# Performance work log

Measured on AMD Instinct MI355X. Metric: run time of the kernel, lower is better.

## Reference

```python
import jax, jax.numpy as jnp
import numpy as np

N_IN, N_OUT, K, G = 128, 128, 3, 8
BATCH = 512
GRID_MIN, GRID_MAX = -1.0, 1.0
EDGES = N_IN * N_OUT


def setup_inputs() -> dict:
    key = jax.random.key(0)
    k1, k2 = jax.random.split(key)
    # inputs inside the grid range so splines are active
    x = jax.random.uniform(k1, (BATCH, N_IN), dtype=jnp.float32,
                           minval=GRID_MIN, maxval=GRID_MAX)
    # per-edge extended uniform knot vector: G+2K+1 points (k extra on each side)
    h = (GRID_MAX - GRID_MIN) / G
    knots_1d = jnp.linspace(GRID_MIN - K * h, GRID_MAX + K * h,
                            G + 2 * K + 1, dtype=jnp.float32)
    knots = jnp.broadcast_to(knots_1d, (EDGES, G + 2 * K + 1))
    c_basis = (jax.random.normal(k2, (EDGES, G + K), dtype=jnp.float32) * 0.1)
    c_spl = jnp.ones((N_OUT, N_IN), jnp.float32)
    c_res = jnp.ones((N_OUT, N_IN), jnp.float32)
    bias = jnp.zeros((N_OUT,), jnp.float32)
    return {"x": x, "knots": knots, "c_basis": c_basis,
            "c_spl": c_spl, "c_res": c_res, "bias": bias}


def _extend(x):
    # (batch, n_in) -> (edges, batch) with edge index = o*n_in + i
    batch = x.shape[0]
    return jnp.broadcast_to(x[:, None, :], (batch, N_OUT, N_IN)).reshape(batch, EDGES).T


def _basis(x, knots):
    # Cox-de Boor recursion; returns (edges, G+K, batch)
    x_ext = _extend(x)                   # (edges, batch)
    grid = knots[:, :, None]             # (edges, G+2K+1, 1)
    x_in = x_ext[:, None, :]             # (edges, 1, batch)
    b = ((x_in >= grid[:, :-1]) & (x_in < grid[:, 1:])).astype(jnp.float32)
    for order in range(1, K + 1):
        left = (x_in - grid[:, :-(order + 1)]) / (grid[:, order:-1] - grid[:, :-(order + 1)])
        right = (grid[:, order + 1:] - x_in) / (grid[:, order + 1:] - grid[:, 1:-order])
        b = left * b[:, :-1] + right * b[:, 1:]
    return b


def reference(x, knots, c_basis, c_spl, c_res, bias):
    batch = x.shape[0]
    bi = _basis(x, knots)                           # (edges, G+K, batch)
    spl = jnp.einsum('eg,egb->eb', c_basis, bi).T   # (batch, edges)
    y = c_spl.reshape(1, EDGES) * spl
    x_ext = _extend(x).T                            # (batch, edges)
    y = y + c_res.reshape(1, EDGES) * jax.nn.silu(x_ext)
    y = jnp.sum(y.reshape(batch, N_OUT, N_IN), axis=2) + bias
    return y
```

## Files before the change

kernel.cpp:

```cpp
#include <hip/hip_runtime.h>
#include <math.h>

#define N_IN  128
#define N_OUT 128
#define BATCH 512
#define NK    11
#define TBV   16
#define TOV   16
#define KTOT  1536
#define ASTR  1544

typedef float f32x4  __attribute__((ext_vector_type(4)));
typedef short bf16x8 __attribute__((ext_vector_type(8)));
typedef unsigned long long u64;

__device__ __forceinline__ unsigned short f2bf(float f) {
    unsigned u = __float_as_uint(f);
    u += 0x7FFFu + ((u >> 16) & 1u);
    return (unsigned short)(u >> 16);
}

__global__ __launch_bounds__(128) void w_pack(
    const float* __restrict__ cbasis, const float* __restrict__ cspl,
    const float* __restrict__ cres, unsigned short* __restrict__ w2)
{
    const int e = blockIdx.x * 128 + threadIdx.x;
    const float s = cspl[e];
    const float* src = cbasis + (size_t)e * NK;
    unsigned short h[12];
    #pragma unroll
    for (int g = 0; g < NK; ++g) h[g] = f2bf(s * src[g]);
    h[11] = f2bf(cres[e]);
    unsigned d[6];
    #pragma unroll
    for (int j = 0; j < 6; ++j)
        d[j] = (unsigned)h[2 * j] | ((unsigned)h[2 * j + 1] << 16);
    unsigned short* dst = w2 + (size_t)e * 12;
    *(uint2*)(dst)     = make_uint2(d[0], d[1]);
    *(uint2*)(dst + 4) = make_uint2(d[2], d[3]);
    *(uint2*)(dst + 8) = make_uint2(d[4], d[5]);
}

__global__ __launch_bounds__(512) void kan_kernel(
    const float* __restrict__ x,
    const unsigned short* __restrict__ w2,
    const float* __restrict__ bias,
    float* __restrict__ y)
{
    __shared__ short sA[TBV * ASTR];
    __shared__ float sAcc[8 * 256];

    const int b0 = blockIdx.x * TBV;
    const int o0 = blockIdx.y * TOV;
    const int t  = threadIdx.x;
    const int w  = t >> 6;
    const int l  = t & 63;
    const int mn = l & 15;
    const int kq = (l >> 4) * 8;

    const unsigned short* wb = w2 + (size_t)(o0 + mn) * KTOT + w * 192 + kq;
    bf16x8 wf[6];
    #pragma unroll
    for (int s = 0; s < 6; ++s)
        wf[s] = *(const bf16x8*)(wb + s * 32);

    float xv[4];
    #pragma unroll
    for (int it = 0; it < 4; ++it) {
        const int p = t + it * 512;
        xv[it] = x[(b0 + (p >> 7)) * N_IN + (p & 127)];
    }
    #pragma unroll
    for (int it = 0; it < 4; ++it) {
        const int p = t + it * 512;
        const int b = p >> 7, i = p & 127;
        const float v = xv[it];
        const float u = (v + 1.75f) * 4.0f;
        float jf = floorf(u);
        jf = fminf(fmaxf(jf, 3.0f), 10.0f);
        const float tt = u - jf;
        const float omt = 1.0f - tt;
        const float t2 = tt * tt, t3 = t2 * tt;
        const float B0 = omt * omt * omt * (1.0f / 6.0f);
        const float B1 = (3.0f * t3 - 6.0f * t2 + 4.0f) * (1.0f / 6.0f);
        const float B2 = (-3.0f * t3 + 3.0f * t2 + 3.0f * tt + 1.0f) * (1.0f / 6.0f);
        const float B3 = t3 * (1.0f / 6.0f);
        const int base = (int)jf - 3;
        const float sig = 1.0f / (1.0f + __expf(-v));
        const u64 v4 = (u64)f2bf(B0) | ((u64)f2bf(B1) << 16)
                     | ((u64)f2bf(B2) << 32) | ((u64)f2bf(B3) << 48);
        const int sh = base * 16;
        u64 q0, q1, q2;
        if (sh < 64) {
            q0 = v4 << sh;
            q1 = sh ? (v4 >> (64 - sh)) : 0ull;
            q2 = 0ull;
        } else {
            q0 = 0ull;
            q1 = v4 << (sh - 64);
            q2 = (sh > 64) ? (v4 >> (128 - sh)) : 0ull;
        }
        q2 |= (u64)f2bf(v * sig) << 48;
        u64* dst = (u64*)&sA[b * ASTR + i * 12];
        dst[0] = q0; dst[1] = q1; dst[2] = q2;
    }
    __syncthreads();

    f32x4 acc = {0.f, 0.f, 0.f, 0.f};
    const short* aB = &sA[mn * ASTR + w * 192 + kq];
    #pragma unroll
    for (int s = 0; s < 6; ++s) {
        bf16x8 af = *(const bf16x8*)(aB + s * 32);
        acc = __builtin_amdgcn_mfma_f32_16x16x32_bf16(af, wf[s], acc, 0, 0, 0);
    }

    #pragma unroll
    for (int r = 0; r < 4; ++r)
        sAcc[w * 256 + ((l >> 4) * 4 + r) * 16 + mn] = acc[r];
    __syncthreads();
    if (t < 256) {
        const int m2 = t >> 4, n2 = t & 15;
        float sum = bias[o0 + n2];
        #pragma unroll
        for (int ww = 0; ww < 8; ++ww) sum += sAcc[ww * 256 + t];
        y[(b0 + m2) * N_OUT + (o0 + n2)] = sum;
    }
}

extern "C" void kernel_launch(void* const* d_in, const int* in_sizes, int n_in,
                              void* d_out, int out_size, void* d_ws, size_t ws_size,
                              hipStream_t stream) {
    const float* x      = (const float*)d_in[0];
    const float* cbasis = (const float*)d_in[2];
    const float* cspl   = (const float*)d_in[3];
    const float* cres   = (const float*)d_in[4];
    const float* bias   = (const float*)d_in[5];
    float* y = (float*)d_out;
    unsigned short* w2 = (unsigned short*)d_ws;

    w_pack<<<128, 128, 0, stream>>>(cbasis, cspl, cres, w2);
    dim3 grid(BATCH / TBV, N_OUT / TOV);
    kan_kernel<<<grid, 512, 0, stream>>>(x, w2, bias, y);
}
```

Measured before the change: 67.11 us.

## Precompute spline basis activations once in pack kernel instead of per output tile

Moves the B-spline basis and SiLU evaluation of x out of the GEMM kernel into the packing kernel, which writes a global bf16 activation matrix alongside the packed weights. Previously each of the 8 output-tile columns recomputed the basis for its batch tile in shared memory; now the GEMM kernel loads both operands directly from global into registers with no shared staging or barrier. This removes redundant transcendental work and a sync, at the cost of an extra global write/read of the activation matrix (about 1.5 MB).

```diff
diff --git a/kernel.cpp b/kernel.cpp
--- a/kernel.cpp
+++ b/kernel.cpp
@@ -8,7 +8,6 @@
 #define TBV   16
 #define TOV   16
 #define KTOT  1536
-#define ASTR  1544
 
 typedef float f32x4  __attribute__((ext_vector_type(4)));
 typedef short bf16x8 __attribute__((ext_vector_type(8)));
@@ -20,61 +19,30 @@
     return (unsigned short)(u >> 16);
 }
 
-__global__ __launch_bounds__(128) void w_pack(
-    const float* __restrict__ cbasis, const float* __restrict__ cspl,
-    const float* __restrict__ cres, unsigned short* __restrict__ w2)
+__global__ __launch_bounds__(256) void pack_kernel(
+    const float* __restrict__ x,      const float* __restrict__ cbasis,
+    const float* __restrict__ cspl,   const float* __restrict__ cres,
+    unsigned short* __restrict__ w2,  unsigned short* __restrict__ a2)
 {
-    const int e = blockIdx.x * 128 + threadIdx.x;
-    const float s = cspl[e];
-    const float* src = cbasis + (size_t)e * NK;
-    unsigned short h[12];
-    #pragma unroll
-    for (int g = 0; g < NK; ++g) h[g] = f2bf(s * src[g]);
-    h[11] = f2bf(cres[e]);
-    unsigned d[6];
-    #pragma unroll
-    for (int j = 0; j < 6; ++j)
-        d[j] = (unsigned)h[2 * j] | ((unsigned)h[2 * j + 1] << 16);
-    unsigned short* dst = w2 + (size_t)e * 12;
-    *(uint2*)(dst)     = make_uint2(d[0], d[1]);
-    *(uint2*)(dst + 4) = make_uint2(d[2], d[3]);
-    *(uint2*)(dst + 8) = make_uint2(d[4], d[5]);
-}
-
-__global__ __launch_bounds__(512) void kan_kernel(
-    const float* __restrict__ x,
-    const unsigned short* __restrict__ w2,
-    const float* __restrict__ bias,
-    float* __restrict__ y)
-{
-    __shared__ short sA[TBV * ASTR];
-    __shared__ float sAcc[8 * 256];
-
-    const int b0 = blockIdx.x * TBV;
-    const int o0 = blockIdx.y * TOV;
-    const int t  = threadIdx.x;
-    const int w  = t >> 6;
-    const int l  = t & 63;
-    const int mn = l & 15;
-    const int kq = (l >> 4) * 8;
-
-    const unsigned short* wb = w2 + (size_t)(o0 + mn) * KTOT + w * 192 + kq;
-    bf16x8 wf[6];
-    #pragma unroll
-    for (int s = 0; s < 6; ++s)
-        wf[s] = *(const bf16x8*)(wb + s * 32);
-
-    float xv[4];
-    #pragma unroll
-    for (int it = 0; it < 4; ++it) {
-        const int p = t + it * 512;
-        xv[it] = x[(b0 + (p >> 7)) * N_IN + (p & 127)];
-    }
-    #pragma unroll
-    for (int it = 0; it < 4; ++it) {
-        const int p = t + it * 512;
-        const int b = p >> 7, i = p & 127;
-        const float v = xv[it];
+    if (blockIdx.x < 64) {
+        const int e = blockIdx.x * 256 + threadIdx.x;
+        const float s = cspl[e];
+        const float* src = cbasis + (size_t)e * NK;
+        unsigned short h[12];
+        #pragma unroll
+        for (int g = 0; g < NK; ++g) h[g] = f2bf(s * src[g]);
+        h[11] = f2bf(cres[e]);
+        unsigned d[6];
+        #pragma unroll
+        for (int j = 0; j < 6; ++j)
+            d[j] = (unsigned)h[2 * j] | ((unsigned)h[2 * j + 1] << 16);
+        unsigned short* dst = w2 + (size_t)e * 12;
+        *(uint2*)(dst)     = make_uint2(d[0], d[1]);
+        *(uint2*)(dst + 4) = make_uint2(d[2], d[3]);
+        *(uint2*)(dst + 8) = make_uint2(d[4], d[5]);
+    } else {
+        const int p = (blockIdx.x - 64) * 256 + threadIdx.x;
+        const float v = x[p];
         const float u = (v + 1.75f) * 4.0f;
         float jf = floorf(u);
         jf = fminf(fmaxf(jf, 3.0f), 10.0f);
@@ -101,18 +69,40 @@
             q2 = (sh > 64) ? (v4 >> (128 - sh)) : 0ull;
         }
         q2 |= (u64)f2bf(v * sig) << 48;
-        u64* dst = (u64*)&sA[b * ASTR + i * 12];
+        u64* dst = (u64*)(a2 + (size_t)p * 12);
         dst[0] = q0; dst[1] = q1; dst[2] = q2;
     }
-    __syncthreads();
+}
+
+__global__ __launch_bounds__(512) void kan_kernel(
+    const unsigned short* __restrict__ a2,
+    const unsigned short* __restrict__ w2,
+    const float* __restrict__ bias,
+    float* __restrict__ y)
+{
+    __shared__ float sAcc[8 * 256];
+
+    const int b0 = blockIdx.x * TBV;
+    const int o0 = blockIdx.y * TOV;
+    const int t  = threadIdx.x;
+    const int w  = t >> 6;
+    const int l  = t & 63;
+    const int mn = l & 15;
+    const int kq = (l >> 4) * 8;
+
+    const unsigned short* ab = a2 + (size_t)(b0 + mn) * KTOT + w * 192 + kq;
+    const unsigned short* wb = w2 + (size_t)(o0 + mn) * KTOT + w * 192 + kq;
+    bf16x8 af[6], wf[6];
+    #pragma unroll
+    for (int s = 0; s < 6; ++s) {
+        af[s] = *(const bf16x8*)(ab + s * 32);
+        wf[s] = *(const bf16x8*)(wb + s * 32);
+    }
 
     f32x4 acc = {0.f, 0.f, 0.f, 0.f};
-    const short* aB = &sA[mn * ASTR + w * 192 + kq];
     #pragma unroll
-    for (int s = 0; s < 6; ++s) {
-        bf16x8 af = *(const bf16x8*)(aB + s * 32);
-        acc = __builtin_amdgcn_mfma_f32_16x16x32_bf16(af, wf[s], acc, 0, 0, 0);
-    }
+    for (int s = 0; s < 6; ++s)
+        acc = __builtin_amdgcn_mfma_f32_16x16x32_bf16(af[s], wf[s], acc, 0, 0, 0);
 
     #pragma unroll
     for (int r = 0; r < 4; ++r)
@@ -137,8 +127,9 @@
     const float* bias   = (const float*)d_in[5];
     float* y = (float*)d_out;
     unsigned short* w2 = (unsigned short*)d_ws;
+    unsigned short* a2 = (unsigned short*)((char*)d_ws + 512 * 1024);
 
-    w_pack<<<128, 128, 0, stream>>>(cbasis, cspl, cres, w2);
+    pack_kernel<<<320, 256, 0, stream>>>(x, cbasis, cspl, cres, w2, a2);
     dim3 grid(BATCH / TBV, N_OUT / TOV);
-    kan_kernel<<<grid, 512, 0, stream>>>(x, w2, bias, y);
+    kan_kernel<<<grid, 512, 0, stream>>>(a2, w2, bias, y);
 }
```

Result: no change. 68.01 us (+1.3%).
